# Kernel tuning notes

Measured on AMD Instinct MI355X. Metric: run time of the kernel, lower is better.

Reference implementation:

```python
import jax, jax.numpy as jnp
import numpy as np
import math


def setup_inputs() -> dict:
    key = jax.random.key(0)
    ks = jax.random.split(key, 5)
    B, C, E = 4, 2048, 1024
    max_len = 2048
    s = 1.0 / math.sqrt(E)
    return {
        "x": jax.random.normal(ks[0], (B, C, E), dtype=jnp.float32),
        "W_q": jax.random.normal(ks[1], (E, E), dtype=jnp.float32) * s,
        "W_k": jax.random.normal(ks[2], (E, E), dtype=jnp.float32) * s,
        "W_v": jax.random.normal(ks[3], (E, E), dtype=jnp.float32) * s,
        "rel_bias": jax.random.normal(ks[4], (2 * max_len - 1, 1), dtype=jnp.float32),
        "max_len": max_len,
    }


def reference(x, W_q, W_k, W_v, rel_bias, max_len):
    B, C, E = x.shape
    # nn.Linear(bias=False): y = x @ W.T
    Q = jnp.einsum("bce,fe->bcf", x, W_q)
    K = jnp.einsum("bce,fe->bcf", x, W_k)
    V = jnp.einsum("bce,fe->bcf", x, W_v)
    scores = jnp.einsum("bqe,bke->bqk", Q, K) / math.sqrt(E)
    pos = jnp.arange(C)
    rel_dist = jnp.clip(pos[None, :] - pos[:, None] + (max_len - 1), 0, 2 * max_len - 2)
    bias = rel_bias[rel_dist, 0]  # [C, C]
    scores = scores + bias[None, :, :]
    weights = jax.nn.softmax(scores, axis=-1)
    out = jnp.einsum("bqk,bke->bqe", weights, V)
    return out, weights
```

## Files before the change

kernel.cpp:

```cpp
#include <hip/hip_runtime.h>
#include <hip/hip_bf16.h>
#include <math.h>

typedef __attribute__((ext_vector_type(8))) short short8;
typedef __attribute__((ext_vector_type(4))) short short4v;
typedef __attribute__((ext_vector_type(4))) float f32x4;

static __device__ __forceinline__ short f2bf(float f) {
  union { float f; unsigned u; } x;
  x.f = f;
  unsigned r = x.u + 0x7fffu + ((x.u >> 16) & 1u);
  return (short)(r >> 16);
}

#define GLD16(g, l)                                                   \
  __builtin_amdgcn_global_load_lds(                                   \
      (const __attribute__((address_space(1))) void*)(g),             \
      (__attribute__((address_space(3))) void*)(l), 16, 0, 0)
#define BAR() asm volatile("s_barrier" ::: "memory")
#define VMCNT3() asm volatile("s_waitcnt vmcnt(3)" ::: "memory")
#define VMCNT0() asm volatile("s_waitcnt vmcnt(0)" ::: "memory")

__global__ __launch_bounds__(256) void cvt_f32_bf16(const float* __restrict__ in,
                                                    short* __restrict__ out, int n8) {
  int i = blockIdx.x * 256 + threadIdx.x;
  if (i >= n8) return;
  const float4* p = (const float4*)in + (size_t)i * 2;
  float4 a = p[0], b = p[1];
  short8 o;
  o[0] = f2bf(a.x); o[1] = f2bf(a.y); o[2] = f2bf(a.z); o[3] = f2bf(a.w);
  o[4] = f2bf(b.x); o[5] = f2bf(b.y); o[6] = f2bf(b.z); o[7] = f2bf(b.w);
  *((short8*)out + i) = o;
}

template <int MODE>
__global__ __launch_bounds__(512) void gemm8p(
    const short* __restrict__ A, const short* __restrict__ Bt,
    void* __restrict__ C0, void* __restrict__ C1, void* __restrict__ C2,
    const float* __restrict__ rel_bias,
    int N, int K, long aZ, long bZ, long cZ, int Cdim, float scale, int ml) {
  __shared__ short sA[2][256 * 64];
  __shared__ short sB[2][128 * 64];
  const int tid = threadIdx.x, lane = tid & 63, wid = tid >> 6;
  const int z = blockIdx.z;
  const short* Az = A + (size_t)z * aZ;
  const short* Bz = Bt + (size_t)z * bZ;
  const int brow = blockIdx.x * 256, bcol = blockIdx.y * 128;
  const int wr = wid >> 2, wc = wid & 3;
  const int lrow = lane & 15, kg = lane >> 4;
  const int l8 = lane >> 3, lm8 = lane & 7;
  const int scol = (lm8 ^ l8) * 8;

  const short* aS[2][2];
  int aD[2][2];
#pragma unroll
  for (int h = 0; h < 2; ++h)
#pragma unroll
    for (int j = 0; j < 2; ++j) {
      int c = wid * 2 + j;
      int rb = c * 8 + (c >= 8 ? 64 : 0) + h * 64;
      aS[h][j] = Az + (size_t)(brow + rb + l8) * K + scol;
      aD[h][j] = rb * 64;
    }
  const short* bS[2];
  int bD[2];
#pragma unroll
  for (int h = 0; h < 2; ++h) {
    int rb = wid * 8 + h * 64;
    bS[h] = Bz + (size_t)(bcol + rb + l8) * K + scol;
    bD[h] = rb * 64;
  }

  const int sks0 = ((0 + kg) ^ (lrow & 7)) * 8;
  const int sks1 = ((4 + kg) ^ (lrow & 7)) * 8;
  const int aR = (wr * 128 + lrow) * 64;
  const int bR = (wc * 32 + lrow) * 64;

  short8 a[4][2], b[2][2];
  f32x4 acc[8][2] = {};

#define STG_A(BUF, H, T)                                          \
  do {                                                            \
    GLD16(aS[H][0] + (size_t)(T) * 64, &sA[BUF][aD[H][0]]);       \
    GLD16(aS[H][1] + (size_t)(T) * 64, &sA[BUF][aD[H][1]]);       \
  } while (0)
#define STG_B(BUF, H, T) GLD16(bS[H] + (size_t)(T) * 64, &sB[BUF][bD[H]])
#define RD_A(BUF, MH)                                                         \
  do {                                                                        \
    _Pragma("unroll") for (int mq = 0; mq < 4; ++mq) {                        \
      a[mq][0] = *(const short8*)&sA[BUF][aR + (MH)*4096 + mq * 1024 + sks0]; \
      a[mq][1] = *(const short8*)&sA[BUF][aR + (MH)*4096 + mq * 1024 + sks1]; \
    }                                                                         \
  } while (0)
#define RD_B(BUF)                                                  \
  do {                                                             \
    _Pragma("unroll") for (int nq = 0; nq < 2; ++nq) {             \
      b[nq][0] = *(const short8*)&sB[BUF][bR + nq * 1024 + sks0];  \
      b[nq][1] = *(const short8*)&sB[BUF][bR + nq * 1024 + sks1];  \
    }                                                              \
  } while (0)
#define MFMA16(MH)                                                            \
  do {                                                                        \
    __builtin_amdgcn_s_setprio(1);                                            \
    _Pragma("unroll") for (int mq = 0; mq < 4; ++mq)                          \
        _Pragma("unroll") for (int nq = 0; nq < 2; ++nq) {                    \
      acc[(MH)*4 + mq][nq] = __builtin_amdgcn_mfma_f32_16x16x32_bf16(         \
          a[mq][0], b[nq][0], acc[(MH)*4 + mq][nq], 0, 0, 0);                 \
      acc[(MH)*4 + mq][nq] = __builtin_amdgcn_mfma_f32_16x16x32_bf16(         \
          a[mq][1], b[nq][1], acc[(MH)*4 + mq][nq], 0, 0, 0);                 \
    }                                                                         \
    __builtin_amdgcn_s_setprio(0);                                            \
  } while (0)

  STG_A(0, 0, 0); STG_B(0, 0, 0); STG_A(0, 1, 0); STG_B(0, 1, 0);
  STG_A(1, 0, 1); STG_B(1, 0, 1);
  VMCNT3();
  BAR();

  const int NIT = K >> 7;
  for (int i = 0; i < NIT - 1; ++i) {
    const int t1 = 2 * i + 1, t2 = 2 * i + 2, t3 = 2 * i + 3;
    RD_A(0, 0); RD_B(0);
    STG_A(1, 1, t1); STG_B(1, 1, t1);
    BAR();
    MFMA16(0);
    BAR();
    RD_A(0, 1);
    STG_A(0, 0, t2); STG_B(0, 0, t2);
    BAR();
    MFMA16(1);
    VMCNT3();
    BAR();
    RD_A(1, 0); RD_B(1);
    STG_A(0, 1, t2); STG_B(0, 1, t2);
    BAR();
    MFMA16(0);
    BAR();
    RD_A(1, 1);
    STG_A(1, 0, t3); STG_B(1, 0, t3);
    BAR();
    MFMA16(1);
    VMCNT3();
    BAR();
  }
  {
    const int t1 = 2 * (NIT - 1) + 1;
    RD_A(0, 0); RD_B(0);
    STG_A(1, 1, t1); STG_B(1, 1, t1);
    BAR(); MFMA16(0); BAR();
    RD_A(0, 1);
    BAR(); MFMA16(1);
    VMCNT0();
    BAR();
    RD_A(1, 0); RD_B(1);
    BAR(); MFMA16(0); BAR();
    RD_A(1, 1);
    BAR(); MFMA16(1);
  }

#pragma unroll
  for (int m = 0; m < 8; ++m) {
#pragma unroll
    for (int n = 0; n < 2; ++n) {
#pragma unroll
      for (int r = 0; r < 4; ++r) {
        float v = acc[m][n][r];
        int gr = brow + wr * 128 + m * 16 + kg * 4 + r;
        int gc = bcol + wc * 32 + n * 16 + lrow;
        if constexpr (MODE == 2) {
          int idx = gc - gr + (ml - 1);
          idx = min(max(idx, 0), 2 * ml - 2);
          ((float*)C0 + (size_t)z * cZ)[(size_t)gr * N + gc] =
              v * scale + rel_bias[idx];
        } else if constexpr (MODE == 3) {
          ((float*)C0 + (size_t)z * cZ)[(size_t)gr * N + gc] = v;
        } else {
          int s = gc >> 10, cc = gc & 1023;
          if (s == 0) {
            ((short*)C0)[(size_t)gr * 1024 + cc] = f2bf(v);
          } else if (s == 1) {
            ((short*)C1)[(size_t)gr * 1024 + cc] = f2bf(v);
          } else {
            int b_ = gr / Cdim, c_ = gr % Cdim;
            ((short*)C2)[((size_t)b_ * 1024 + cc) * Cdim + c_] = f2bf(v);
          }
        }
      }
    }
  }
#undef STG_A
#undef STG_B
#undef RD_A
#undef RD_B
#undef MFMA16
}

__global__ __launch_bounds__(256) void softmax_rows(float* __restrict__ w,
                                                    short* __restrict__ wb, int Cd) {
  const size_t row = blockIdx.x;
  float4* p = (float4*)(w + row * (size_t)Cd);
  const int tid = threadIdx.x;
  float4 v0 = p[tid];
  float4 v1 = p[tid + 256];
  float mx = fmaxf(fmaxf(fmaxf(v0.x, v0.y), fmaxf(v0.z, v0.w)),
                   fmaxf(fmaxf(v1.x, v1.y), fmaxf(v1.z, v1.w)));
#pragma unroll
  for (int o = 32; o; o >>= 1) mx = fmaxf(mx, __shfl_xor(mx, o));
  __shared__ float red[8];
  const int wv = tid >> 6;
  if ((tid & 63) == 0) red[wv] = mx;
  __syncthreads();
  mx = fmaxf(fmaxf(red[0], red[1]), fmaxf(red[2], red[3]));
  v0.x = __expf(v0.x - mx); v0.y = __expf(v0.y - mx);
  v0.z = __expf(v0.z - mx); v0.w = __expf(v0.w - mx);
  v1.x = __expf(v1.x - mx); v1.y = __expf(v1.y - mx);
  v1.z = __expf(v1.z - mx); v1.w = __expf(v1.w - mx);
  float s = v0.x + v0.y + v0.z + v0.w + v1.x + v1.y + v1.z + v1.w;
#pragma unroll
  for (int o = 32; o; o >>= 1) s += __shfl_xor(s, o);
  if ((tid & 63) == 0) red[4 + wv] = s;
  __syncthreads();
  s = red[4] + red[5] + red[6] + red[7];
  float inv = 1.0f / s;
  v0.x *= inv; v0.y *= inv; v0.z *= inv; v0.w *= inv;
  v1.x *= inv; v1.y *= inv; v1.z *= inv; v1.w *= inv;
  p[tid] = v0;
  p[tid + 256] = v1;
  short4v b0, b1;
  b0[0] = f2bf(v0.x); b0[1] = f2bf(v0.y); b0[2] = f2bf(v0.z); b0[3] = f2bf(v0.w);
  b1[0] = f2bf(v1.x); b1[1] = f2bf(v1.y); b1[2] = f2bf(v1.z); b1[3] = f2bf(v1.w);
  short* wrow = wb + row * (size_t)Cd;
  *(short4v*)&wrow[tid * 4] = b0;
  *(short4v*)&wrow[1024 + tid * 4] = b1;
}

extern "C" void kernel_launch(void* const* d_in, const int* in_sizes, int n_in,
                              void* d_out, int out_size, void* d_ws, size_t ws_size,
                              hipStream_t stream) {
  const float* x = (const float*)d_in[0];
  const float* Wq = (const float*)d_in[1];
  const float* Wk = (const float*)d_in[2];
  const float* Wv = (const float*)d_in[3];
  const float* rb = (const float*)d_in[4];

  const int E = 1024;
  const int Mt = in_sizes[0] / E;
  const int Cd = out_size / Mt - E;
  const int B = Mt / Cd;
  const int ml = (in_sizes[4] + 1) / 2;
  const float scale = 1.0f / sqrtf((float)E);

  short* xb = (short*)d_ws;
  short* wqb = xb + (size_t)Mt * E;
  short* wkb = wqb + (size_t)E * E;
  short* wvb = wkb + (size_t)E * E;
  short* Qb = wvb + (size_t)E * E;
  short* Kb = Qb + (size_t)Mt * E;
  short* Vt = Kb + (size_t)Mt * E;
  short* wbf = Qb;

  float* outp = (float*)d_out;
  float* wts = outp + (size_t)Mt * E;

  cvt_f32_bf16<<<(Mt * E) / 2048, 256, 0, stream>>>(x, xb, (Mt * E) / 8);
  cvt_f32_bf16<<<(E * E) / 2048, 256, 0, stream>>>(Wq, wqb, (E * E) / 8);
  cvt_f32_bf16<<<(E * E) / 2048, 256, 0, stream>>>(Wk, wkb, (E * E) / 8);
  cvt_f32_bf16<<<(E * E) / 2048, 256, 0, stream>>>(Wv, wvb, (E * E) / 8);

  dim3 blk(512);
  gemm8p<4><<<dim3(Mt / 256, 3 * E / 128, 1), blk, 0, stream>>>(
      xb, wqb, Qb, Kb, Vt, nullptr, 3 * E, E, 0, 0, 0, Cd, 0.f, ml);
  gemm8p<2><<<dim3(Cd / 256, Cd / 128, B), blk, 0, stream>>>(
      Qb, Kb, wts, nullptr, nullptr, rb, Cd, E, (long)Cd * E, (long)Cd * E,
      (long)Cd * Cd, Cd, scale, ml);
  softmax_rows<<<Mt, 256, 0, stream>>>(wts, wbf, Cd);
  gemm8p<3><<<dim3(Cd / 256, E / 128, B), blk, 0, stream>>>(
      wbf, Vt, outp, nullptr, nullptr, nullptr, E, Cd, (long)Cd * Cd,
      (long)E * Cd, (long)Cd * E, Cd, 0.f, ml);
}
```

Measured before the change: 214.2 us.

## Switch GEMM pipeline from double to triple-buffered LDS with rotating pointers

Moves the GEMM mainloop from a two-buffer LDS scheme to three rotating buffers. Each K tile is now prefetched two steps ahead, with vmcnt(6) keeping more global loads in flight. The unrolled two-tile body becomes a single-tile loop that rotates buffer pointers each iteration. LDS use rises to 144 KB per block, which may limit occupancy, and runtime pointer rotation may cost addressing registers.

```diff
diff --git a/kernel.cpp b/kernel.cpp
--- a/kernel.cpp
+++ b/kernel.cpp
@@ -18,7 +18,7 @@
       (const __attribute__((address_space(1))) void*)(g),             \
       (__attribute__((address_space(3))) void*)(l), 16, 0, 0)
 #define BAR() asm volatile("s_barrier" ::: "memory")
-#define VMCNT3() asm volatile("s_waitcnt vmcnt(3)" ::: "memory")
+#define VMCNT6() asm volatile("s_waitcnt vmcnt(6)" ::: "memory")
 #define VMCNT0() asm volatile("s_waitcnt vmcnt(0)" ::: "memory")
 
 __global__ __launch_bounds__(256) void cvt_f32_bf16(const float* __restrict__ in,
@@ -34,13 +34,13 @@
 }
 
 template <int MODE>
-__global__ __launch_bounds__(512) void gemm8p(
+__global__ __launch_bounds__(512) void gemm3b(
     const short* __restrict__ A, const short* __restrict__ Bt,
     void* __restrict__ C0, void* __restrict__ C1, void* __restrict__ C2,
     const float* __restrict__ rel_bias,
     int N, int K, long aZ, long bZ, long cZ, int Cdim, float scale, int ml) {
-  __shared__ short sA[2][256 * 64];
-  __shared__ short sB[2][128 * 64];
+  __shared__ short sA[3][256 * 64];
+  __shared__ short sB[3][128 * 64];
   const int tid = threadIdx.x, lane = tid & 63, wid = tid >> 6;
   const int z = blockIdx.z;
   const short* Az = A + (size_t)z * aZ;
@@ -79,24 +79,27 @@
   short8 a[4][2], b[2][2];
   f32x4 acc[8][2] = {};
 
-#define STG_A(BUF, H, T)                                          \
-  do {                                                            \
-    GLD16(aS[H][0] + (size_t)(T) * 64, &sA[BUF][aD[H][0]]);       \
-    GLD16(aS[H][1] + (size_t)(T) * 64, &sA[BUF][aD[H][1]]);       \
-  } while (0)
-#define STG_B(BUF, H, T) GLD16(bS[H] + (size_t)(T) * 64, &sB[BUF][bD[H]])
-#define RD_A(BUF, MH)                                                         \
+  short *pa0 = &sA[0][0], *pa1 = &sA[1][0], *pa2 = &sA[2][0];
+  short *pb0 = &sB[0][0], *pb1 = &sB[1][0], *pb2 = &sB[2][0];
+
+#define STG_A(PA, H, T)                                          \
+  do {                                                           \
+    GLD16(aS[H][0] + (size_t)(T) * 64, (PA) + aD[H][0]);         \
+    GLD16(aS[H][1] + (size_t)(T) * 64, (PA) + aD[H][1]);         \
+  } while (0)
+#define STG_B(PB, H, T) GLD16(bS[H] + (size_t)(T) * 64, (PB) + bD[H])
+#define RD_A(PA, MH)                                                          \
   do {                                                                        \
     _Pragma("unroll") for (int mq = 0; mq < 4; ++mq) {                        \
-      a[mq][0] = *(const short8*)&sA[BUF][aR + (MH)*4096 + mq * 1024 + sks0]; \
-      a[mq][1] = *(const short8*)&sA[BUF][aR + (MH)*4096 + mq * 1024 + sks1]; \
+      a[mq][0] = *(const short8*)&(PA)[aR + (MH)*4096 + mq * 1024 + sks0];    \
+      a[mq][1] = *(const short8*)&(PA)[aR + (MH)*4096 + mq * 1024 + sks1];    \
     }                                                                         \
   } while (0)
-#define RD_B(BUF)                                                  \
+#define RD_B(PB)                                                   \
   do {                                                             \
     _Pragma("unroll") for (int nq = 0; nq < 2; ++nq) {             \
-      b[nq][0] = *(const short8*)&sB[BUF][bR + nq * 1024 + sks0];  \
-      b[nq][1] = *(const short8*)&sB[BUF][bR + nq * 1024 + sks1];  \
+      b[nq][0] = *(const short8*)&(PB)[bR + nq * 1024 + sks0];     \
+      b[nq][1] = *(const short8*)&(PB)[bR + nq * 1024 + sks1];     \
     }                                                              \
   } while (0)
 #define MFMA16(MH)                                                            \
@@ -112,51 +115,37 @@
     __builtin_amdgcn_s_setprio(0);                                            \
   } while (0)
 
-  STG_A(0, 0, 0); STG_B(0, 0, 0); STG_A(0, 1, 0); STG_B(0, 1, 0);
-  STG_A(1, 0, 1); STG_B(1, 0, 1);
-  VMCNT3();
+  STG_A(pa0, 0, 0); STG_B(pb0, 0, 0); STG_A(pa0, 1, 0); STG_B(pb0, 1, 0);
+  STG_A(pa1, 0, 1); STG_B(pb1, 0, 1); STG_A(pa1, 1, 1); STG_B(pb1, 1, 1);
+  VMCNT6();
   BAR();
 
-  const int NIT = K >> 7;
-  for (int i = 0; i < NIT - 1; ++i) {
-    const int t1 = 2 * i + 1, t2 = 2 * i + 2, t3 = 2 * i + 3;
-    RD_A(0, 0); RD_B(0);
-    STG_A(1, 1, t1); STG_B(1, 1, t1);
+  const int NT = K >> 6;
+  for (int t = 0; t < NT - 2; ++t) {
+    RD_A(pa0, 0); RD_B(pb0);
+    STG_A(pa2, 0, t + 2); STG_B(pb2, 0, t + 2);
     BAR();
     MFMA16(0);
     BAR();
-    RD_A(0, 1);
-    STG_A(0, 0, t2); STG_B(0, 0, t2);
+    RD_A(pa0, 1);
+    STG_A(pa2, 1, t + 2); STG_B(pb2, 1, t + 2);
+    VMCNT6();
     BAR();
     MFMA16(1);
-    VMCNT3();
-    BAR();
-    RD_A(1, 0); RD_B(1);
-    STG_A(0, 1, t2); STG_B(0, 1, t2);
-    BAR();
-    MFMA16(0);
-    BAR();
-    RD_A(1, 1);
-    STG_A(1, 0, t3); STG_B(1, 0, t3);
-    BAR();
-    MFMA16(1);
-    VMCNT3();
-    BAR();
+    BAR();
+    short* q;
+    q = pa0; pa0 = pa1; pa1 = pa2; pa2 = q;
+    q = pb0; pb0 = pb1; pb1 = pb2; pb2 = q;
   }
-  {
-    const int t1 = 2 * (NIT - 1) + 1;
-    RD_A(0, 0); RD_B(0);
-    STG_A(1, 1, t1); STG_B(1, 1, t1);
-    BAR(); MFMA16(0); BAR();
-    RD_A(0, 1);
-    BAR(); MFMA16(1);
-    VMCNT0();
-    BAR();
-    RD_A(1, 0); RD_B(1);
-    BAR(); MFMA16(0); BAR();
-    RD_A(1, 1);
-    BAR(); MFMA16(1);
-  }
+  RD_A(pa0, 0); RD_B(pb0);
+  BAR(); MFMA16(0); BAR();
+  RD_A(pa0, 1);
+  VMCNT0();
+  BAR(); MFMA16(1); BAR();
+  RD_A(pa1, 0); RD_B(pb1);
+  BAR(); MFMA16(0); BAR();
+  RD_A(pa1, 1);
+  BAR(); MFMA16(1);
 
 #pragma unroll
   for (int m = 0; m < 8; ++m) {
@@ -268,13 +257,13 @@
   cvt_f32_bf16<<<(E * E) / 2048, 256, 0, stream>>>(Wv, wvb, (E * E) / 8);
 
   dim3 blk(512);
-  gemm8p<4><<<dim3(Mt / 256, 3 * E / 128, 1), blk, 0, stream>>>(
+  gemm3b<4><<<dim3(Mt / 256, 3 * E / 128, 1), blk, 0, stream>>>(
       xb, wqb, Qb, Kb, Vt, nullptr, 3 * E, E, 0, 0, 0, Cd, 0.f, ml);
-  gemm8p<2><<<dim3(Cd / 256, Cd / 128, B), blk, 0, stream>>>(
+  gemm3b<2><<<dim3(Cd / 256, Cd / 128, B), blk, 0, stream>>>(
       Qb, Kb, wts, nullptr, nullptr, rb, Cd, E, (long)Cd * E, (long)Cd * E,
       (long)Cd * Cd, Cd, scale, ml);
   softmax_rows<<<Mt, 256, 0, stream>>>(wts, wbf, Cd);
-  gemm8p<3><<<dim3(Cd / 256, E / 128, B), blk, 0, stream>>>(
+  gemm3b<3><<<dim3(Cd / 256, E / 128, B), blk, 0, stream>>>(
       wbf, Vt, outp, nullptr, nullptr, nullptr, E, Cd, (long)Cd * Cd,
       (long)E * Cd, (long)Cd * E, Cd, 0.f, ml);
 }
```

After: 209.2 us. -2.4%, faster.
